# Optimization experiments

Measured on AMD Instinct MI355X. Metric: run time of the kernel, lower is better.

The kernel has to match this reference:

```python
import jax, jax.numpy as jnp
import numpy as np

K = 64
M = 256
V = 5000

def setup_inputs() -> dict:
    key = jax.random.key(0)
    ks = jax.random.split(key, 8)
    feat_x = jax.random.normal(ks[0], (1, V, M), dtype=jnp.float32)
    feat_y = jax.random.normal(ks[1], (1, V, M), dtype=jnp.float32)
    evals_x = jnp.sort(jax.random.uniform(ks[2], (1, K), dtype=jnp.float32))
    evals_y = jnp.sort(jax.random.uniform(ks[3], (1, K), dtype=jnp.float32))
    evecs_trans_x = jax.random.normal(ks[4], (1, K, V), dtype=jnp.float32) / np.sqrt(V)
    evecs_trans_y = jax.random.normal(ks[5], (1, K, V), dtype=jnp.float32) / np.sqrt(V)
    eye = jnp.eye(K, dtype=jnp.float32)
    sqrtMk_x = (eye + 0.05 * jax.random.normal(ks[6], (K, K), dtype=jnp.float32))[None]
    sqrtMk_y = (eye + 0.05 * jax.random.normal(ks[7], (K, K), dtype=jnp.float32))[None]
    return {"feat_x": feat_x, "feat_y": feat_y, "evals_x": evals_x, "evals_y": evals_y,
            "evecs_trans_x": evecs_trans_x, "evecs_trans_y": evecs_trans_y,
            "sqrtMk_x": sqrtMk_x, "sqrtMk_y": sqrtMk_y}

LMBDA = 0.001

def _fmap(fx, fy, ex, ey, tx, ty, sx, sy):
    # squeeze batch dim of 1 (as in torch .squeeze())
    fx, fy = fx[0], fy[0]            # [V, m]
    ex, ey = ex[0], ey[0]            # [k]
    tx, ty = tx[0], ty[0]            # [k, V]
    sx, sy = sx[0], sy[0]            # [k, k]
    A = tx @ fx                      # [k, m] spectral coeffs of feat_x
    B = sy @ (ty @ fy)               # adapt_feature=True: premultiply by sqrtMk_y
    k, m = A.shape
    vec_B = B.T.reshape(m * k, 1)
    At_Ik = jnp.kron(A.T, sy)        # [m*k, k*k] (adapt_feature -> Ik = sqrtMk_y)
    first = At_Ik.T @ At_Ik          # [k^2, k^2]
    # adapt_mask=True branch
    inv_sx = jnp.linalg.inv(sx)
    lx = jnp.diag(ex)
    ly = jnp.diag(ey)
    lx_Ik = jnp.kron(lx @ inv_sx, sy)
    Ik_ly = jnp.kron(inv_sx, sy @ ly)
    Delta = lx_Ik - Ik_ly
    second = Delta.T @ Delta
    rhs = At_Ik.T @ vec_B
    op = first + LMBDA * second
    C = jnp.linalg.solve(op, rhs)
    return C.reshape(k, k).T[None]   # [1, k, k]

def reference(feat_x, feat_y, evals_x, evals_y, evecs_trans_x, evecs_trans_y, sqrtMk_x, sqrtMk_y):
    # bidirectional=False -> only Cxy (Cyx is None in the torch module)
    return _fmap(feat_x, feat_y, evals_x, evals_y, evecs_trans_x, evecs_trans_y, sqrtMk_x, sqrtMk_y)
```

## Files before the change

kernel.cpp:

```cpp
#include <hip/hip_runtime.h>

#define LMBDA 0.001f
#define NS_SY 4
#define NS_G  5
#define NS_SX 5
#define OUTER 3
#define LDP 68
#define GYS 30

#define WS_A    0
#define WS_FY   16384
#define WS_G1   32768
#define WS_FYAT 36864
#define WS_T1   40960
#define WS_R2   45056
#define WS_R4   49152
#define WS_C    53248
#define WS_FLAGS 57344

#define FMA4(ar, xs, b) { ar[0]=fmaf((xs),(b).x,ar[0]); ar[1]=fmaf((xs),(b).y,ar[1]); \
                          ar[2]=fmaf((xs),(b).z,ar[2]); ar[3]=fmaf((xs),(b).w,ar[3]); }

template<int SA, int SB>
__device__ __forceinline__ void mm64(const float* __restrict__ A,
                                     const float* __restrict__ B,
                                     int ti, int tj, float a[4][4]) {
    #pragma unroll 4
    for (int k = 0; k < 64; k += 4) {
        float4 av0 = *(const float4*)&A[(4 * ti + 0) * SA + k];
        float4 av1 = *(const float4*)&A[(4 * ti + 1) * SA + k];
        float4 av2 = *(const float4*)&A[(4 * ti + 2) * SA + k];
        float4 av3 = *(const float4*)&A[(4 * ti + 3) * SA + k];
        float4 b0 = *(const float4*)&B[(k + 0) * SB + 4 * tj];
        float4 b1 = *(const float4*)&B[(k + 1) * SB + 4 * tj];
        float4 b2 = *(const float4*)&B[(k + 2) * SB + 4 * tj];
        float4 b3 = *(const float4*)&B[(k + 3) * SB + 4 * tj];
        FMA4(a[0], av0.x, b0); FMA4(a[0], av0.y, b1); FMA4(a[0], av0.z, b2); FMA4(a[0], av0.w, b3);
        FMA4(a[1], av1.x, b0); FMA4(a[1], av1.y, b1); FMA4(a[1], av1.z, b2); FMA4(a[1], av1.w, b3);
        FMA4(a[2], av2.x, b0); FMA4(a[2], av2.y, b1); FMA4(a[2], av2.z, b2); FMA4(a[2], av2.w, b3);
        FMA4(a[3], av3.x, b0); FMA4(a[3], av3.y, b1); FMA4(a[3], av3.z, b2); FMA4(a[3], av3.w, b3);
    }
}

template<int SA, int SB>
__device__ __forceinline__ void mmdot(const float* __restrict__ A,
                                      const float* __restrict__ B,
                                      int ti, int tj, float a[4][4]) {
    #pragma unroll 4
    for (int m = 0; m < 64; m += 4) {
        float4 av[4], bv[4];
        #pragma unroll
        for (int r = 0; r < 4; ++r) av[r] = *(const float4*)&A[(4 * ti + r) * SA + m];
        #pragma unroll
        for (int c = 0; c < 4; ++c) bv[c] = *(const float4*)&B[(4 * tj + c) * SB + m];
        #pragma unroll
        for (int r = 0; r < 4; ++r)
            #pragma unroll
            for (int c = 0; c < 4; ++c)
                a[r][c] += av[r].x * bv[c].x + av[r].y * bv[c].y
                         + av[r].z * bv[c].z + av[r].w * bv[c].w;
    }
}

template<int SM>
__device__ __forceinline__ void ns_invert(const float* sM, float* sX, float* sY,
                                          int iters, int ti, int tj,
                                          int tid, float alpha)
{
    const float a2 = alpha * alpha;
    for (int idx = tid; idx < 4096; idx += 256) {
        int i = idx >> 6, j = idx & 63;
        sX[i * LDP + j] = ((i == j) ? 2.f * alpha : 0.f) - a2 * sM[i * SM + j];
    }
    __syncthreads();
    for (int it = 1; it < iters; ++it) {
        float y[4][4] = {};
        mm64<SM, LDP>(sM, sX, ti, tj, y);
        #pragma unroll
        for (int r = 0; r < 4; ++r) {
            float4 v = {y[r][0], y[r][1], y[r][2], y[r][3]};
            *(float4*)&sY[(4 * ti + r) * 64 + 4 * tj] = v;
        }
        __syncthreads();
        float z[4][4] = {};
        mm64<LDP, 64>(sX, sY, ti, tj, z);
        __syncthreads();
        #pragma unroll
        for (int r = 0; r < 4; ++r) {
            float4 xv = *(const float4*)&sX[(4 * ti + r) * LDP + 4 * tj];
            xv.x = 2.f * xv.x - z[r][0];
            xv.y = 2.f * xv.y - z[r][1];
            xv.z = 2.f * xv.z - z[r][2];
            xv.w = 2.f * xv.w - z[r][3];
            *(float4*)&sX[(4 * ti + r) * LDP + 4 * tj] = xv;
        }
        __syncthreads();
    }
}

__device__ __forceinline__ void wait_ge(int* flag, int target, int tid) {
    if (tid == 0) {
        while (__hip_atomic_load(flag, __ATOMIC_ACQUIRE, __HIP_MEMORY_SCOPE_AGENT) < target)
            __builtin_amdgcn_s_sleep(8);
    }
    __syncthreads();
    __threadfence();
}

__device__ __forceinline__ void signal_one(int* flag, int tid) {
    __syncthreads();
    __threadfence();
    if (tid == 0)
        (void)__hip_atomic_fetch_add(flag, 1, __ATOMIC_RELEASE, __HIP_MEMORY_SCOPE_AGENT);
}

__global__ __launch_bounds__(256, 1) void fused_fmnet(
    const float* __restrict__ fx, const float* __restrict__ fy,
    const float* __restrict__ ex, const float* __restrict__ ey,
    const float* __restrict__ tx, const float* __restrict__ ty,
    const float* __restrict__ sx, const float* __restrict__ sy,
    float* __restrict__ ws, float* __restrict__ out)
{
    extern __shared__ __align__(16) float lds[];
    int* flags = (int*)(ws + WS_FLAGS);
    const int tid = threadIdx.x;
    const int ti = tid >> 4, tj = tid & 15;
    const int bid = blockIdx.x;

    if (bid < 240) {
        float* sT = lds;
        float* sF = lds + 4352;
        const int gx = bid & 7, gy = bid >> 3;
        const int mat = gx >> 2;
        const int m0 = (gx & 3) << 6;
        const float* __restrict__ T = mat ? ty : tx;
        const float* __restrict__ F = mat ? fy : fx;
        float* __restrict__ Out = ws + (mat ? WS_FY : WS_A);

        float4 tv[4], fv[4];
        int sc = gy;
        int vlen = 5000 - (sc << 6); if (vlen > 64) vlen = 64;
        #pragma unroll
        for (int w = 0; w < 4; ++w) {
            const int fidx = tid + (w << 8);
            const int row = fidx >> 4, q = fidx & 15, vv = q << 2;
            if (vv < vlen) tv[w] = *(const float4*)(T + (size_t)row * 5000 + (sc << 6) + vv);
            if (row < vlen) fv[w] = *(const float4*)(F + (size_t)((sc << 6) + row) * 256 + m0 + (q << 2));
        }
        #pragma unroll
        for (int w = 0; w < 4; ++w) {
            const int fidx = tid + (w << 8);
            const int row = fidx >> 4, q = fidx & 15, vv = q << 2;
            if (vv < vlen) {
                sT[(vv + 0) * LDP + row] = tv[w].x;
                sT[(vv + 1) * LDP + row] = tv[w].y;
                sT[(vv + 2) * LDP + row] = tv[w].z;
                sT[(vv + 3) * LDP + row] = tv[w].w;
            }
            if (row < vlen) *(float4*)&sF[row * LDP + (q << 2)] = fv[w];
        }
        __syncthreads();

        float acc[4][4] = {};
        for (;;) {
            const int nsc = sc + GYS;
            int nvlen = 5000 - (nsc << 6);
            if (nvlen > 64) nvlen = 64;
            if (nvlen > 0) {
                #pragma unroll
                for (int w = 0; w < 4; ++w) {
                    const int fidx = tid + (w << 8);
                    const int row = fidx >> 4, q = fidx & 15, vv = q << 2;
                    if (vv < nvlen) tv[w] = *(const float4*)(T + (size_t)row * 5000 + (nsc << 6) + vv);
                    if (row < nvlen) fv[w] = *(const float4*)(F + (size_t)((nsc << 6) + row) * 256 + m0 + (q << 2));
                }
            }
            #pragma unroll 4
            for (int v = 0; v < vlen; ++v) {
                float4 av = *(const float4*)&sT[v * LDP + 4 * ti];
                float4 bv = *(const float4*)&sF[v * LDP + 4 * tj];
                FMA4(acc[0], av.x, bv); FMA4(acc[1], av.y, bv);
                FMA4(acc[2], av.z, bv); FMA4(acc[3], av.w, bv);
            }
            if (nvlen <= 0) break;
            __syncthreads();
            #pragma unroll
            for (int w = 0; w < 4; ++w) {
                const int fidx = tid + (w << 8);
                const int row = fidx >> 4, q = fidx & 15, vv = q << 2;
                if (vv < nvlen) {
                    sT[(vv + 0) * LDP + row] = tv[w].x;
                    sT[(vv + 1) * LDP + row] = tv[w].y;
                    sT[(vv + 2) * LDP + row] = tv[w].z;
                    sT[(vv + 3) * LDP + row] = tv[w].w;
                }
                if (row < nvlen) *(float4*)&sF[row * LDP + (q << 2)] = fv[w];
            }
            __syncthreads();
            sc = nsc; vlen = nvlen;
        }
        #pragma unroll
        for (int r = 0; r < 4; ++r)
            #pragma unroll
            for (int c = 0; c < 4; ++c)
                atomicAdd(&Out[(4 * ti + r) * 256 + m0 + 4 * tj + c], acc[r][c]);
        __syncthreads();
        __threadfence();
        if (tid == 0)
            (void)__hip_atomic_fetch_add(&flags[gx], 1, __ATOMIC_RELEASE, __HIP_MEMORY_SCOPE_AGENT);
    } else if (bid < 244) {
        const int ch = bid - 240;
        wait_ge(&flags[ch], GYS, tid);
        float* sA = lds;
        for (int idx = tid; idx < 1024; idx += 256) {
            int i = idx >> 4, m4 = (idx & 15) << 2;
            *(float4*)&sA[i * LDP + m4] =
                *(const float4*)&ws[WS_A + i * 256 + (ch << 6) + m4];
        }
        __syncthreads();
        float a[4][4] = {};
        mmdot<LDP, LDP>(sA, sA, ti, tj, a);
        #pragma unroll
        for (int r = 0; r < 4; ++r)
            #pragma unroll
            for (int c = 0; c < 4; ++c)
                atomicAdd(&ws[WS_G1 + (4 * ti + r) * 64 + 4 * tj + c], a[r][c]);
        __syncthreads();
        __threadfence();
        if (tid == 0)
            (void)__hip_atomic_fetch_add(&flags[8], 1, __ATOMIC_RELEASE, __HIP_MEMORY_SCOPE_AGENT);
    } else if (bid < 248) {
        const int ch = bid - 244;
        wait_ge(&flags[ch], GYS, tid);
        wait_ge(&flags[4 + ch], GYS, tid);
        float* sFy = lds;
        float* sAx = lds + 4352;
        for (int idx = tid; idx < 1024; idx += 256) {
            int i = idx >> 4, m4 = (idx & 15) << 2;
            *(float4*)&sFy[i * LDP + m4] = *(const float4*)&ws[WS_FY + i * 256 + (ch << 6) + m4];
            *(float4*)&sAx[i * LDP + m4] = *(const float4*)&ws[WS_A  + i * 256 + (ch << 6) + m4];
        }
        __syncthreads();
        float a[4][4] = {};
        mmdot<LDP, LDP>(sFy, sAx, ti, tj, a);
        #pragma unroll
        for (int r = 0; r < 4; ++r)
            #pragma unroll
            for (int c = 0; c < 4; ++c)
                atomicAdd(&ws[WS_FYAT + (4 * ti + r) * 64 + 4 * tj + c], a[r][c]);
        signal_one(&flags[9], tid);
    } else if (bid == 248) {
        float* sSy = lds;
        float* sXx = lds + 4352;
        float* sYy = lds + 8704;
        float* sH  = lds + 12800;
        float* sV  = lds + 16896;
        for (int idx = tid; idx < 1024; idx += 256) {
            int i = idx >> 4, j4 = (idx & 15) << 2;
            *(float4*)&sSy[i * LDP + j4] = *(const float4*)&sy[i * 64 + j4];
        }
        if (tid < 64) sV[tid] = ey[tid];
        __syncthreads();
        {
            float h[4][4] = {};
            for (int k = 0; k < 64; ++k) {
                float4 av = *(const float4*)&sSy[k * LDP + 4 * ti];
                float4 bv = *(const float4*)&sSy[k * LDP + 4 * tj];
                FMA4(h[0], av.x, bv); FMA4(h[1], av.y, bv);
                FMA4(h[2], av.z, bv); FMA4(h[3], av.w, bv);
            }
            #pragma unroll
            for (int r = 0; r < 4; ++r) {
                float4 v = {h[r][0], h[r][1], h[r][2], h[r][3]};
                *(float4*)&sH[(4 * ti + r) * 64 + 4 * tj] = v;
            }
        }
        __syncthreads();
        ns_invert<LDP>(sSy, sXx, sYy, NS_SY, ti, tj, tid, 1.0f);
        {
            float h[4][4] = {};
            mmdot<LDP, LDP>(sXx, sXx, ti, tj, h);
            __syncthreads();
            #pragma unroll
            for (int r = 0; r < 4; ++r) {
                float4 v = {h[r][0], h[r][1], h[r][2], h[r][3]};
                *(float4*)&sSy[(4 * ti + r) * LDP + 4 * tj] = v;
            }
        }
        __syncthreads();
        {
            float a[4][4] = {};
            #pragma unroll 4
            for (int k = 0; k < 64; k += 4) {
                float4 av[4];
                #pragma unroll
                for (int r = 0; r < 4; ++r) av[r] = *(const float4*)&sSy[(4 * ti + r) * LDP + k];
                #pragma unroll
                for (int q = 0; q < 4; ++q) {
                    float e = sV[k + q];
                    float4 bv = *(const float4*)&sH[(k + q) * 64 + 4 * tj];
                    bv.x *= e; bv.y *= e; bv.z *= e; bv.w *= e;
                    float xq[4] = {av[0].x, av[1].x, av[2].x, av[3].x};
                    if (q == 1) { xq[0]=av[0].y; xq[1]=av[1].y; xq[2]=av[2].y; xq[3]=av[3].y; }
                    if (q == 2) { xq[0]=av[0].z; xq[1]=av[1].z; xq[2]=av[2].z; xq[3]=av[3].z; }
                    if (q == 3) { xq[0]=av[0].w; xq[1]=av[1].w; xq[2]=av[2].w; xq[3]=av[3].w; }
                    #pragma unroll
                    for (int r = 0; r < 4; ++r) FMA4(a[r], xq[r], bv);
                }
            }
            #pragma unroll
            for (int r = 0; r < 4; ++r) {
                float4 v = {a[r][0], a[r][1], a[r][2], a[r][3]};
                *(float4*)&ws[WS_C + (4 * ti + r) * 64 + 4 * tj] = v;
            }
        }
        signal_one(&flags[9], tid);
    } else if (bid == 249) {
        float* sM = lds;
        float* sX = lds + 4352;
        float* sY = lds + 8704;
        float* sV = lds + 12800;
        for (int idx = tid; idx < 1024; idx += 256) {
            int i = idx >> 4, j4 = (idx & 15) << 2;
            *(float4*)&sM[i * LDP + j4] = *(const float4*)&sx[i * 64 + j4];
        }
        if (tid < 64) sV[tid] = ex[tid];
        __syncthreads();
        ns_invert<LDP>(sM, sX, sY, NS_SX, ti, tj, tid, 1.0f);
        float aR2[4][4] = {}, aR4[4][4] = {}, aT1[4][4] = {};
        for (int k = 0; k < 64; ++k) {
            float e = sV[k], e2 = e * e;
            float4 av = *(const float4*)&sX[k * LDP + 4 * ti];
            float4 bv = *(const float4*)&sX[k * LDP + 4 * tj];
            float avv[4] = {av.x, av.y, av.z, av.w};
            #pragma unroll
            for (int r = 0; r < 4; ++r) {
                FMA4(aR4[r], avv[r], bv);
                float ea = e * avv[r];
                FMA4(aR2[r], ea, bv);
                float e2a = e2 * avv[r];
                FMA4(aT1[r], e2a, bv);
            }
        }
        #pragma unroll
        for (int r = 0; r < 4; ++r) {
            int o = (4 * ti + r) * 64 + 4 * tj;
            float4 v2 = {aR2[r][0], aR2[r][1], aR2[r][2], aR2[r][3]};
            float4 v4 = {aR4[r][0], aR4[r][1], aR4[r][2], aR4[r][3]};
            float4 v1 = {aT1[r][0], aT1[r][1], aT1[r][2], aT1[r][3]};
            *(float4*)&ws[WS_R2 + o] = v2;
            *(float4*)&ws[WS_R4 + o] = v4;
            *(float4*)&ws[WS_T1 + o] = v1;
        }
        signal_one(&flags[9], tid);
    } else {
        float* cM1   = lds;
        float* cR2   = lds + 4096;
        float* cR4   = lds + 8192;
        float* cGinv = lds + 12288;
        float* sE    = lds + 16384;
        float* sX    = lds + 20480;
        float* cC    = lds + 24832;
        float* sW    = lds + 29184;

        wait_ge(&flags[8], 4, tid);
        for (int idx = tid; idx < 1024; idx += 256) {
            int i = idx >> 4, j4 = (idx & 15) << 2;
            *(float4*)&cM1[i * 64 + j4] = *(const float4*)&ws[WS_G1 + i * 64 + j4];
        }
        __syncthreads();
        if (tid < 64) {
            float s = 0.f;
            for (int j4 = 0; j4 < 64; j4 += 4) {
                float4 v = *(const float4*)&cM1[tid * 64 + j4];
                s += v.x * v.x + v.y * v.y + v.z * v.z + v.w * v.w;
            }
            sW[tid] = s;
            sW[64 + tid] = cM1[tid * 64 + tid];
        }
        __syncthreads();
        float f2 = 0.f, tr = 0.f;
        for (int i = 0; i < 64; ++i) { f2 += sW[i]; tr += sW[64 + i]; }
        ns_invert<64>(cM1, sX, sE, NS_G, ti, tj, tid, tr / f2);
        for (int idx = tid; idx < 1024; idx += 256) {
            int i = idx >> 4, j4 = (idx & 15) << 2;
            *(float4*)&cGinv[i * 64 + j4] = *(const float4*)&sX[i * LDP + j4];
        }
        wait_ge(&flags[9], 6, tid);
        for (int idx = tid; idx < 1024; idx += 256) {
            int i = idx >> 4, j4 = (idx & 15) << 2;
            int o = i * 64 + j4;
            float4 gv = *(const float4*)&cM1[o];
            float4 t = *(const float4*)&ws[WS_T1 + o];
            gv.x = fmaf(LMBDA, t.x, gv.x); gv.y = fmaf(LMBDA, t.y, gv.y);
            gv.z = fmaf(LMBDA, t.z, gv.z); gv.w = fmaf(LMBDA, t.w, gv.w);
            *(float4*)&cM1[o] = gv;
            *(float4*)&cR2[o] = *(const float4*)&ws[WS_R2 + o];
            *(float4*)&cR4[o] = *(const float4*)&ws[WS_R4 + o];
            *(float4*)&cC[i * LDP + j4] = *(const float4*)&ws[WS_C + o];
        }
        float4 eyv = *(const float4*)&ey[4 * ti];
        float eyr[4] = {eyv.x, eyv.y, eyv.z, eyv.w};
        float leyr[4];
        #pragma unroll
        for (int r = 0; r < 4; ++r) leyr[r] = LMBDA * eyr[r];

        float fyr[4][4], xreg[4][4];
        #pragma unroll
        for (int r = 0; r < 4; ++r) {
            float4 v = *(const float4*)&ws[WS_FYAT + (4 * ti + r) * 64 + 4 * tj];
            fyr[r][0] = v.x; fyr[r][1] = v.y; fyr[r][2] = v.z; fyr[r][3] = v.w;
            float4 z = {0.f, 0.f, 0.f, 0.f};
            *(float4*)&sX[(4 * ti + r) * LDP + 4 * tj] = z;
            #pragma unroll
            for (int c = 0; c < 4; ++c) xreg[r][c] = 0.f;
        }
        __syncthreads();

        float E1[4][4];
        for (int it = 0; it < OUTER; ++it) {
            {
                float Sm[4][4] = {}, S2[4][4] = {}, S4[4][4] = {};
                #pragma unroll 2
                for (int k = 0; k < 64; k += 4) {
                    float4 av[4];
                    #pragma unroll
                    for (int r = 0; r < 4; ++r)
                        av[r] = *(const float4*)&sX[(4 * ti + r) * LDP + k];
                    #pragma unroll
                    for (int q = 0; q < 4; ++q) {
                        float4 mv = *(const float4*)&cM1[(k + q) * 64 + 4 * tj];
                        float4 qv = *(const float4*)&cR2[(k + q) * 64 + 4 * tj];
                        float4 rv = *(const float4*)&cR4[(k + q) * 64 + 4 * tj];
                        float xq[4] = {av[0].x, av[1].x, av[2].x, av[3].x};
                        if (q == 1) { xq[0]=av[0].y; xq[1]=av[1].y; xq[2]=av[2].y; xq[3]=av[3].y; }
                        if (q == 2) { xq[0]=av[0].z; xq[1]=av[1].z; xq[2]=av[2].z; xq[3]=av[3].z; }
                        if (q == 3) { xq[0]=av[0].w; xq[1]=av[1].w; xq[2]=av[2].w; xq[3]=av[3].w; }
                        #pragma unroll
                        for (int r = 0; r < 4; ++r) {
                            FMA4(Sm[r], xq[r], mv);
                            FMA4(S2[r], xq[r], qv);
                            FMA4(S4[r], xq[r], rv);
                        }
                    }
                }
                #pragma unroll
                for (int r = 0; r < 4; ++r) {
                    float4 e2;
                    e2.x = LMBDA * fmaf(eyr[r], S4[r][0], -S2[r][0]);
                    e2.y = LMBDA * fmaf(eyr[r], S4[r][1], -S2[r][1]);
                    e2.z = LMBDA * fmaf(eyr[r], S4[r][2], -S2[r][2]);
                    e2.w = LMBDA * fmaf(eyr[r], S4[r][3], -S2[r][3]);
                    *(float4*)&sE[(4 * ti + r) * 64 + 4 * tj] = e2;
                    #pragma unroll
                    for (int c = 0; c < 4; ++c)
                        E1[r][c] = fmaf(-leyr[r], S2[r][c], Sm[r][c]);
                }
            }
            __syncthreads();
            {
                float Z[4][4] = {};
                mm64<LDP, 64>(cC, sE, ti, tj, Z);
                #pragma unroll
                for (int r = 0; r < 4; ++r) {
                    float4 w;
                    w.x = fyr[r][0] - E1[r][0] - Z[r][0];
                    w.y = fyr[r][1] - E1[r][1] - Z[r][1];
                    w.z = fyr[r][2] - E1[r][2] - Z[r][2];
                    w.w = fyr[r][3] - E1[r][3] - Z[r][3];
                    *(float4*)&sW[(4 * ti + r) * LDP + 4 * tj] = w;
                }
            }
            __syncthreads();
            {
                float dX[4][4] = {};
                mm64<LDP, 64>(sW, cGinv, ti, tj, dX);
                #pragma unroll
                for (int r = 0; r < 4; ++r) {
                    float4 v;
                    #pragma unroll
                    for (int c = 0; c < 4; ++c) xreg[r][c] += dX[r][c];
                    v.x = xreg[r][0]; v.y = xreg[r][1]; v.z = xreg[r][2]; v.w = xreg[r][3];
                    *(float4*)&sX[(4 * ti + r) * LDP + 4 * tj] = v;
                    if (it == OUTER - 1)
                        *(float4*)&out[(4 * ti + r) * 64 + 4 * tj] = v;
                }
            }
            if (it == OUTER - 1) break;
            __syncthreads();
        }
    }
}

extern "C" void kernel_launch(void* const* d_in, const int* in_sizes, int n_in,
                              void* d_out, int out_size, void* d_ws, size_t ws_size,
                              hipStream_t stream) {
    (void)in_sizes; (void)n_in; (void)out_size; (void)ws_size;
    const float* fx = (const float*)d_in[0];
    const float* fy = (const float*)d_in[1];
    const float* ex = (const float*)d_in[2];
    const float* ey = (const float*)d_in[3];
    const float* tx = (const float*)d_in[4];
    const float* ty = (const float*)d_in[5];
    const float* sx = (const float*)d_in[6];
    const float* sy = (const float*)d_in[7];
    float* ws = (float*)d_ws;
    float* out = (float*)d_out;

    (void)hipFuncSetAttribute((const void*)fused_fmnet,
                              hipFuncAttributeMaxDynamicSharedMemorySize, 134144);

    (void)hipMemsetAsync(d_ws, 0, (size_t)(WS_T1) * sizeof(float), stream);
    (void)hipMemsetAsync((char*)d_ws + (size_t)WS_FLAGS * sizeof(float), 0, 64, stream);
    fused_fmnet<<<251, 256, 134144, stream>>>(fx, fy, ex, ey, tx, ty, sx, sy, ws, out);
}
```

Before: 182.1 us.

## Restructure Gram inverse as Neumann-series passes and shortcut first outer iteration

Replaces the generic Newton-Schulz inversion of the Gram matrix with a reformulated series: it builds I - alpha*G, squares it, and runs four fused passes that update the inverse estimate and residual power together. The first outer refinement iteration, which starts from X=0, is replaced by a single matmul of fyAt with the approximate inverse, so only two full correction iterations remain. This cuts serial matmuls on the critical single-block solver path. The LDS buffers are reorganised to fit the new scheme, and approximation accuracy now depends on the series depth and the shortened iteration count.

```diff
diff --git a/kernel.cpp b/kernel.cpp
--- a/kernel.cpp
+++ b/kernel.cpp
@@ -2,9 +2,8 @@
 
 #define LMBDA 0.001f
 #define NS_SY 4
-#define NS_G  5
 #define NS_SX 5
-#define OUTER 3
+#define OUTER_FULL 2
 #define LDP 68
 #define GYS 30
 
@@ -20,6 +19,7 @@
 
 #define FMA4(ar, xs, b) { ar[0]=fmaf((xs),(b).x,ar[0]); ar[1]=fmaf((xs),(b).y,ar[1]); \
                           ar[2]=fmaf((xs),(b).z,ar[2]); ar[3]=fmaf((xs),(b).w,ar[3]); }
+#define COMP(v,q) ((q)==0?(v).x:((q)==1?(v).y:((q)==2?(v).z:(v).w)))
 
 template<int SA, int SB>
 __device__ __forceinline__ void mm64(const float* __restrict__ A,
@@ -98,6 +98,43 @@
     }
 }
 
+template<bool DOR>
+__device__ __forceinline__ void ns_pass(const float* Xs, const float* Rs,
+                                        float* Xd, float* Rd, int ti, int tj)
+{
+    float xr[4][4] = {}, rr[4][4] = {};
+    #pragma unroll 4
+    for (int k = 0; k < 64; k += 4) {
+        float4 xa[4], ra[4];
+        #pragma unroll
+        for (int r = 0; r < 4; ++r) {
+            xa[r] = *(const float4*)&Xs[(4 * ti + r) * LDP + k];
+            if (DOR) ra[r] = *(const float4*)&Rs[(4 * ti + r) * LDP + k];
+        }
+        #pragma unroll
+        for (int q = 0; q < 4; ++q) {
+            float4 bv = *(const float4*)&Rs[(k + q) * LDP + 4 * tj];
+            #pragma unroll
+            for (int r = 0; r < 4; ++r) {
+                FMA4(xr[r], COMP(xa[r], q), bv);
+                if (DOR) FMA4(rr[r], COMP(ra[r], q), bv);
+            }
+        }
+    }
+    #pragma unroll
+    for (int r = 0; r < 4; ++r) {
+        float4 xo = *(const float4*)&Xs[(4 * ti + r) * LDP + 4 * tj];
+        float4 xn = {xo.x + xr[r][0], xo.y + xr[r][1],
+                     xo.z + xr[r][2], xo.w + xr[r][3]};
+        *(float4*)&Xd[(4 * ti + r) * LDP + 4 * tj] = xn;
+        if (DOR) {
+            float4 rv = {rr[r][0], rr[r][1], rr[r][2], rr[r][3]};
+            *(float4*)&Rd[(4 * ti + r) * LDP + 4 * tj] = rv;
+        }
+    }
+    __syncthreads();
+}
+
 __device__ __forceinline__ void wait_ge(int* flag, int target, int tid) {
     if (tid == 0) {
         while (__hip_atomic_load(flag, __ATOMIC_ACQUIRE, __HIP_MEMORY_SCOPE_AGENT) < target)
@@ -300,12 +337,8 @@
                     float e = sV[k + q];
                     float4 bv = *(const float4*)&sH[(k + q) * 64 + 4 * tj];
                     bv.x *= e; bv.y *= e; bv.z *= e; bv.w *= e;
-                    float xq[4] = {av[0].x, av[1].x, av[2].x, av[3].x};
-                    if (q == 1) { xq[0]=av[0].y; xq[1]=av[1].y; xq[2]=av[2].y; xq[3]=av[3].y; }
-                    if (q == 2) { xq[0]=av[0].z; xq[1]=av[1].z; xq[2]=av[2].z; xq[3]=av[3].z; }
-                    if (q == 3) { xq[0]=av[0].w; xq[1]=av[1].w; xq[2]=av[2].w; xq[3]=av[3].w; }
                     #pragma unroll
-                    for (int r = 0; r < 4; ++r) FMA4(a[r], xq[r], bv);
+                    for (int r = 0; r < 4; ++r) FMA4(a[r], COMP(av[r], q), bv);
                 }
             }
             #pragma unroll
@@ -354,50 +387,69 @@
         }
         signal_one(&flags[9], tid);
     } else {
-        float* cM1   = lds;
-        float* cR2   = lds + 4096;
-        float* cR4   = lds + 8192;
-        float* cGinv = lds + 12288;
-        float* sE    = lds + 16384;
-        float* sX    = lds + 20480;
-        float* cC    = lds + 24832;
-        float* sW    = lds + 29184;
+        float* sM  = lds;
+        float* P1  = lds + 4096;
+        float* P2  = lds + 8448;
+        float* P3  = lds + 12800;
+        float* P4  = lds + 17152;
+        float* cR2 = lds + 21504;
+        float* cR4 = lds + 25600;
 
         wait_ge(&flags[8], 4, tid);
         for (int idx = tid; idx < 1024; idx += 256) {
             int i = idx >> 4, j4 = (idx & 15) << 2;
-            *(float4*)&cM1[i * 64 + j4] = *(const float4*)&ws[WS_G1 + i * 64 + j4];
+            *(float4*)&sM[i * 64 + j4] = *(const float4*)&ws[WS_G1 + i * 64 + j4];
         }
         __syncthreads();
         if (tid < 64) {
             float s = 0.f;
             for (int j4 = 0; j4 < 64; j4 += 4) {
-                float4 v = *(const float4*)&cM1[tid * 64 + j4];
+                float4 v = *(const float4*)&sM[tid * 64 + j4];
                 s += v.x * v.x + v.y * v.y + v.z * v.z + v.w * v.w;
             }
-            sW[tid] = s;
-            sW[64 + tid] = cM1[tid * 64 + tid];
+            P1[tid] = s;
+            P1[64 + tid] = sM[tid * 64 + tid];
         }
         __syncthreads();
         float f2 = 0.f, tr = 0.f;
-        for (int i = 0; i < 64; ++i) { f2 += sW[i]; tr += sW[64 + i]; }
-        ns_invert<64>(cM1, sX, sE, NS_G, ti, tj, tid, tr / f2);
-        for (int idx = tid; idx < 1024; idx += 256) {
-            int i = idx >> 4, j4 = (idx & 15) << 2;
-            *(float4*)&cGinv[i * 64 + j4] = *(const float4*)&sX[i * LDP + j4];
-        }
+        for (int i = 0; i < 64; ++i) { f2 += P1[i]; tr += P1[64 + i]; }
+        const float alpha = tr / f2, a2 = alpha * alpha;
+        for (int idx = tid; idx < 4096; idx += 256) {
+            int i = idx >> 6, j = idx & 63;
+            float g = sM[i * 64 + j];
+            float d = (i == j) ? 1.f : 0.f;
+            P3[i * LDP + j] = 2.f * alpha * d - a2 * g;
+            P2[i * LDP + j] = d - alpha * g;
+        }
+        __syncthreads();
+        {
+            float z[4][4] = {};
+            mm64<LDP, LDP>(P2, P2, ti, tj, z);
+            #pragma unroll
+            for (int r = 0; r < 4; ++r) {
+                float4 v = {z[r][0], z[r][1], z[r][2], z[r][3]};
+                *(float4*)&P1[(4 * ti + r) * LDP + 4 * tj] = v;
+            }
+            __syncthreads();
+        }
+        ns_pass<true >(P3, P1, P4, P2, ti, tj);
+        ns_pass<true >(P4, P2, P3, P1, ti, tj);
+        ns_pass<true >(P3, P1, P4, P2, ti, tj);
+        ns_pass<false>(P4, P2, P3, P3, ti, tj);
+
         wait_ge(&flags[9], 6, tid);
         for (int idx = tid; idx < 1024; idx += 256) {
             int i = idx >> 4, j4 = (idx & 15) << 2;
             int o = i * 64 + j4;
-            float4 gv = *(const float4*)&cM1[o];
+            float4 gv = *(const float4*)&sM[o];
             float4 t = *(const float4*)&ws[WS_T1 + o];
             gv.x = fmaf(LMBDA, t.x, gv.x); gv.y = fmaf(LMBDA, t.y, gv.y);
             gv.z = fmaf(LMBDA, t.z, gv.z); gv.w = fmaf(LMBDA, t.w, gv.w);
-            *(float4*)&cM1[o] = gv;
+            *(float4*)&sM[o] = gv;
             *(float4*)&cR2[o] = *(const float4*)&ws[WS_R2 + o];
             *(float4*)&cR4[o] = *(const float4*)&ws[WS_R4 + o];
-            *(float4*)&cC[i * LDP + j4] = *(const float4*)&ws[WS_C + o];
+            *(float4*)&P2[i * LDP + j4] = *(const float4*)&ws[WS_C + o];
+            *(float4*)&P1[i * LDP + j4] = *(const float4*)&ws[WS_FYAT + o];
         }
         float4 eyv = *(const float4*)&ey[4 * ti];
         float eyr[4] = {eyv.x, eyv.y, eyv.z, eyv.w};
@@ -410,15 +462,24 @@
         for (int r = 0; r < 4; ++r) {
             float4 v = *(const float4*)&ws[WS_FYAT + (4 * ti + r) * 64 + 4 * tj];
             fyr[r][0] = v.x; fyr[r][1] = v.y; fyr[r][2] = v.z; fyr[r][3] = v.w;
-            float4 z = {0.f, 0.f, 0.f, 0.f};
-            *(float4*)&sX[(4 * ti + r) * LDP + 4 * tj] = z;
-            #pragma unroll
-            for (int c = 0; c < 4; ++c) xreg[r][c] = 0.f;
+        }
+        __syncthreads();
+
+        {
+            float dX[4][4] = {};
+            mm64<LDP, LDP>(P1, P3, ti, tj, dX);
+            #pragma unroll
+            for (int r = 0; r < 4; ++r) {
+                #pragma unroll
+                for (int c = 0; c < 4; ++c) xreg[r][c] = dX[r][c];
+                float4 v = {xreg[r][0], xreg[r][1], xreg[r][2], xreg[r][3]};
+                *(float4*)&P4[(4 * ti + r) * LDP + 4 * tj] = v;
+            }
         }
         __syncthreads();
 
         float E1[4][4];
-        for (int it = 0; it < OUTER; ++it) {
+        for (int it = 0; it < OUTER_FULL; ++it) {
             {
                 float Sm[4][4] = {}, S2[4][4] = {}, S4[4][4] = {};
                 #pragma unroll 2
@@ -426,24 +487,22 @@
                     float4 av[4];
                     #pragma unroll
                     for (int r = 0; r < 4; ++r)
-                        av[r] = *(const float4*)&sX[(4 * ti + r) * LDP + k];
+                        av[r] = *(const float4*)&P4[(4 * ti + r) * LDP + k];
                     #pragma unroll
                     for (int q = 0; q < 4; ++q) {
-                        float4 mv = *(const float4*)&cM1[(k + q) * 64 + 4 * tj];
+                        float4 mv = *(const float4*)&sM[(k + q) * 64 + 4 * tj];
                         float4 qv = *(const float4*)&cR2[(k + q) * 64 + 4 * tj];
                         float4 rv = *(const float4*)&cR4[(k + q) * 64 + 4 * tj];
-                        float xq[4] = {av[0].x, av[1].x, av[2].x, av[3].x};
-                        if (q == 1) { xq[0]=av[0].y; xq[1]=av[1].y; xq[2]=av[2].y; xq[3]=av[3].y; }
-                        if (q == 2) { xq[0]=av[0].z; xq[1]=av[1].z; xq[2]=av[2].z; xq[3]=av[3].z; }
-                        if (q == 3) { xq[0]=av[0].w; xq[1]=av[1].w; xq[2]=av[2].w; xq[3]=av[3].w; }
                         #pragma unroll
                         for (int r = 0; r < 4; ++r) {
-                            FMA4(Sm[r], xq[r], mv);
-                            FMA4(S2[r], xq[r], qv);
-                            FMA4(S4[r], xq[r], rv);
+                            float x = COMP(av[r], q);
+                            FMA4(Sm[r], x, mv);
+                            FMA4(S2[r], x, qv);
+                            FMA4(S4[r], x, rv);
                         }
                     }
                 }
+                __syncthreads();
                 #pragma unroll
                 for (int r = 0; r < 4; ++r) {
                     float4 e2;
@@ -451,7 +510,7 @@
                     e2.y = LMBDA * fmaf(eyr[r], S4[r][1], -S2[r][1]);
                     e2.z = LMBDA * fmaf(eyr[r], S4[r][2], -S2[r][2]);
                     e2.w = LMBDA * fmaf(eyr[r], S4[r][3], -S2[r][3]);
-                    *(float4*)&sE[(4 * ti + r) * 64 + 4 * tj] = e2;
+                    *(float4*)&P1[(4 * ti + r) * LDP + 4 * tj] = e2;
                     #pragma unroll
                     for (int c = 0; c < 4; ++c)
                         E1[r][c] = fmaf(-leyr[r], S2[r][c], Sm[r][c]);
@@ -460,7 +519,8 @@
             __syncthreads();
             {
                 float Z[4][4] = {};
-                mm64<LDP, 64>(cC, sE, ti, tj, Z);
+                mm64<LDP, LDP>(P2, P1, ti, tj, Z);
+                __syncthreads();
                 #pragma unroll
                 for (int r = 0; r < 4; ++r) {
                     float4 w;
@@ -468,25 +528,25 @@
                     w.y = fyr[r][1] - E1[r][1] - Z[r][1];
                     w.z = fyr[r][2] - E1[r][2] - Z[r][2];
                     w.w = fyr[r][3] - E1[r][3] - Z[r][3];
-                    *(float4*)&sW[(4 * ti + r) * LDP + 4 * tj] = w;
+                    *(float4*)&P1[(4 * ti + r) * LDP + 4 * tj] = w;
                 }
             }
             __syncthreads();
             {
                 float dX[4][4] = {};
-                mm64<LDP, 64>(sW, cGinv, ti, tj, dX);
+                mm64<LDP, LDP>(P1, P3, ti, tj, dX);
                 #pragma unroll
                 for (int r = 0; r < 4; ++r) {
                     float4 v;
                     #pragma unroll
                     for (int c = 0; c < 4; ++c) xreg[r][c] += dX[r][c];
                     v.x = xreg[r][0]; v.y = xreg[r][1]; v.z = xreg[r][2]; v.w = xreg[r][3];
-                    *(float4*)&sX[(4 * ti + r) * LDP + 4 * tj] = v;
-                    if (it == OUTER - 1)
+                    *(float4*)&P4[(4 * ti + r) * LDP + 4 * tj] = v;
+                    if (it == OUTER_FULL - 1)
                         *(float4*)&out[(4 * ti + r) * 64 + 4 * tj] = v;
                 }
             }
-            if (it == OUTER - 1) break;
+            if (it == OUTER_FULL - 1) break;
             __syncthreads();
         }
     }
```

Measured after the change: 170.6 us. 6.3% less time.
